# Optimization experiments

Hardware: AMD Instinct MI355X
Metric: run time of the kernel (lower is better)

The kernel has to match this reference:

```python
import jax, jax.numpy as jnp
import numpy as np

N = 50000    # nodes
E = 640000   # edges (avg degree ~12.8)
IN_NF = 64   # raw atom features
D = 96       # hidden dim
H = 4 * D    # 384
L = 4        # RPETConv layers
G = 512      # graphs in the batch
NOUT = 2


def setup_inputs():
    key = jax.random.key(0)
    ks = iter(jax.random.split(key, 64))
    def lin(shape):
        fi = shape[-2]
        return jax.random.normal(next(ks), shape, jnp.float32) / np.float32(np.sqrt(fi))
    inp = {}
    inp['x'] = jax.random.normal(next(ks), (N, IN_NF), jnp.float32)
    inp['edge_attr'] = jax.random.normal(next(ks), (E, D), jnp.float32)
    inp['emb_W1'] = lin((IN_NF, H)); inp['emb_b1'] = jnp.zeros((H,), jnp.float32)
    inp['emb_W2'] = lin((H, D));     inp['emb_b2'] = jnp.zeros((D,), jnp.float32)
    for nm in ('Wq', 'Wk', 'Wv', 'ffn_W1', 'ffn_W2'):
        inp[nm] = lin((L, D, D))
    for nm in ('bq', 'bk', 'bv', 'ffn_b1', 'ffn_b2', 'n1_b', 'n2_b'):
        inp[nm] = jnp.zeros((L, D), jnp.float32)
    inp['n1_g'] = jnp.ones((L, D), jnp.float32)
    inp['n2_g'] = jnp.ones((L, D), jnp.float32)
    inp['u_W1'] = lin((D, H)); inp['u_b1'] = jnp.zeros((H,), jnp.float32)
    inp['u_W2'] = lin((H, H)); inp['u_b2'] = jnp.zeros((H,), jnp.float32)
    inp['u_g'] = jnp.ones((H,), jnp.float32); inp['u_b'] = jnp.zeros((H,), jnp.float32)
    inp['clf_W'] = lin((H, NOUT)); inp['clf_b'] = jnp.zeros((NOUT,), jnp.float32)
    inp['rec_W1'] = lin((H, H)); inp['rec_b1'] = jnp.zeros((H,), jnp.float32)
    inp['rec_W2'] = lin((H, IN_NF)); inp['rec_b2'] = jnp.zeros((IN_NF,), jnp.float32)
    inp['edge_index'] = jax.random.randint(next(ks), (2, E), 0, N, jnp.int32)
    inp['batch_index'] = jnp.sort(jax.random.randint(next(ks), (N,), 0, G, jnp.int32))
    return inp


def _ln(x, g, b):
    # torch.nn.LayerNorm, eps=1e-5
    m = x.mean(-1, keepdims=True)
    v = ((x - m) ** 2).mean(-1, keepdims=True)
    return (x - m) * jax.lax.rsqrt(v + 1e-5) * g + b


def _forward(fs, edge_index, batch_index):
    (x, edge_attr, emb_W1, emb_b1, emb_W2, emb_b2,
     Wq, bq, Wk, bk, Wv, bv, n1_g, n1_b,
     ffn_W1, ffn_b1, ffn_W2, ffn_b2, n2_g, n2_b,
     u_W1, u_b1, u_W2, u_b2, u_g, u_b,
     clf_W, clf_b, rec_W1, rec_b1, rec_W2, rec_b2) = fs
    src, dst = edge_index[0], edge_index[1]  # PyG: x_j = x[src], x_i = x[dst]
    scale = D ** -0.5
    # atom embedding MLP
    h = jax.nn.relu(x @ emb_W1 + emb_b1) @ emb_W2 + emb_b2  # [N, D]
    for l in range(L):
        x_i = h[dst]                  # [E, D] target gather
        px = h[src] + edge_attr       # [E, D] source + relative positional edge attr
        q = x_i @ Wq[l] + bq[l]
        k = px @ Wk[l] + bk[l]
        v = px @ Wv[l] + bv[l]
        ae = jnp.exp((q * k).sum(-1) * scale)  # [E] (original uses raw exp, no max-sub)
        # faithful quirk: softmax denominator segmented over SOURCE index
        s = ae / jax.ops.segment_sum(ae, src, num_segments=N)[src]
        # aggregation (aggr='add') goes to TARGET index
        agg = jax.ops.segment_sum(s[:, None] * v, dst, num_segments=N)  # [N, D]
        h1 = _ln(h + agg, n1_g[l], n1_b[l])
        f = jax.nn.elu(h1 @ ffn_W1[l] + ffn_b1[l]) @ ffn_W2[l] + ffn_b2[l]
        h = _ln(f + h1, n2_g[l], n2_b[l])
    # updim
    u = jax.nn.leaky_relu(h @ u_W1 + u_b1, 0.01) @ u_W2 + u_b2
    u = _ln(u, u_g, u_b)              # [N, H]
    # mean readout per graph
    cnt = jnp.maximum(jax.ops.segment_sum(jnp.ones((N,), u.dtype), batch_index, num_segments=G), 1.0)
    pooled = jax.ops.segment_sum(u, batch_index, num_segments=G) / cnt[:, None]  # [G, H]
    out = pooled @ clf_W + clf_b      # [G, NOUT]
    r = jax.nn.relu(u @ rec_W1 + rec_b1) @ rec_W2 + rec_b2  # [N, IN_NF]
    return (out, r)


def reference(x, edge_attr, emb_W1, emb_b1, emb_W2, emb_b2, Wq, bq, Wk, bk, Wv, bv, n1_g, n1_b, ffn_W1, ffn_b1, ffn_W2, ffn_b2, n2_g, n2_b, u_W1, u_b1, u_W2, u_b2, u_g, u_b, clf_W, clf_b, rec_W1, rec_b1, rec_W2, rec_b2, edge_index, batch_index):
    fs = (x, edge_attr, emb_W1, emb_b1, emb_W2, emb_b2, Wq, bq, Wk, bk, Wv, bv, n1_g, n1_b,
          ffn_W1, ffn_b1, ffn_W2, ffn_b2, n2_g, n2_b, u_W1, u_b1, u_W2, u_b2, u_g, u_b,
          clf_W, clf_b, rec_W1, rec_b1, rec_W2, rec_b2)
    return _forward(fs, edge_index, batch_index)
```

## Files before the change

### kernel.cpp

```cpp
#include <hip/hip_runtime.h>
#include <math.h>

#define N_NODES 50000
#define N_EDGES 640000
#define INF_ 64
#define DD 96
#define HH 384
#define NLAYERS 4
#define NGRAPH 512
#define NOUT_ 2
#define MAXDEG 64

#define ACT_NONE 0
#define ACT_RELU 1
#define ACT_ELU 2
#define ACT_LEAKY 3

typedef unsigned int uint;
typedef unsigned short ushort;
typedef __attribute__((ext_vector_type(8))) short v8s;
typedef __attribute__((ext_vector_type(4))) float v4f;

__device__ __forceinline__ float bf_lo(uint u) { return __uint_as_float(u << 16); }
__device__ __forceinline__ float bf_hi(uint u) { return __uint_as_float(u & 0xffff0000u); }
__device__ __forceinline__ float bfs(ushort s) { return __uint_as_float(((uint)s) << 16); }
__device__ __forceinline__ ushort f2bf(float f)
{
    uint u = __float_as_uint(f);
    return (ushort)((u + 0x7fffu + ((u >> 16) & 1u)) >> 16);
}

template<int BN, int ACT, bool ACCUM, bool OUT16>
__global__ __launch_bounds__(256)
void gemm_mf(const ushort* __restrict__ A, const ushort* __restrict__ Bt,
             const float* __restrict__ bias, float* __restrict__ C32,
             ushort* __restrict__ C16, int M, int Nc, int K)
{
    const int BM = 128, LDA = 40;
    const int FN = BN / 32;
    __shared__ ushort As[BM * LDA];
    __shared__ ushort Bs[BN * LDA];
    int tid = threadIdx.x;
    int lane = tid & 63, wave = tid >> 6;
    int ln15 = lane & 15, quad = lane >> 4;
    int wm = (wave >> 1) * 64, wn = (wave & 1) * (BN / 2);
    int bm0 = blockIdx.x * BM, bn0 = blockIdx.y * BN;

    v4f acc[4][FN];
    #pragma unroll
    for (int i = 0; i < 4; i++)
        #pragma unroll
        for (int j = 0; j < FN; j++) acc[i][j] = (v4f){0.f, 0.f, 0.f, 0.f};

    for (int k0 = 0; k0 < K; k0 += 32) {
        #pragma unroll
        for (int it = 0; it < 2; it++) {
            int u = it * 256 + tid;
            int r = u >> 2, c8 = (u & 3) * 8;
            int row = bm0 + r;
            int4 v = make_int4(0, 0, 0, 0);
            if (row < M) v = *(const int4*)&A[(size_t)row * K + k0 + c8];
            *(int4*)&As[r * LDA + c8] = v;
        }
        #pragma unroll
        for (int it = 0; it < (BN * 4 + 255) / 256; it++) {
            int u = it * 256 + tid;
            if ((BN * 4) % 256 == 0 || u < BN * 4) {
                int r = u >> 2, c8 = (u & 3) * 8;
                *(int4*)&Bs[r * LDA + c8] =
                    *(const int4*)&Bt[(size_t)(bn0 + r) * K + k0 + c8];
            }
        }
        __syncthreads();
        v8s af[4], bf[FN];
        #pragma unroll
        for (int i = 0; i < 4; i++)
            af[i] = *(const v8s*)&As[(wm + i * 16 + ln15) * LDA + quad * 8];
        #pragma unroll
        for (int j = 0; j < FN; j++)
            bf[j] = *(const v8s*)&Bs[(wn + j * 16 + ln15) * LDA + quad * 8];
        #pragma unroll
        for (int i = 0; i < 4; i++)
            #pragma unroll
            for (int j = 0; j < FN; j++)
                acc[i][j] = __builtin_amdgcn_mfma_f32_16x16x32_bf16(
                    af[i], bf[j], acc[i][j], 0, 0, 0);
        __syncthreads();
    }
    #pragma unroll
    for (int i = 0; i < 4; i++) {
        #pragma unroll
        for (int j = 0; j < FN; j++) {
            int col = bn0 + wn + j * 16 + ln15;
            float bsv = bias ? bias[col] : 0.f;
            #pragma unroll
            for (int r = 0; r < 4; r++) {
                int row = bm0 + wm + i * 16 + quad * 4 + r;
                if (row >= M) continue;
                float v = acc[i][j][r] + bsv;
                if (ACCUM) v += C32[(size_t)row * Nc + col];
                if (ACT == ACT_RELU)       v = fmaxf(v, 0.f);
                else if (ACT == ACT_ELU)   v = v > 0.f ? v : expm1f(v);
                else if (ACT == ACT_LEAKY) v = v > 0.f ? v : 0.01f * v;
                if (OUT16) C16[(size_t)row * Nc + col] = f2bf(v);
                else       C32[(size_t)row * Nc + col] = v;
            }
        }
    }
}

template<bool ACC32>
__global__ __launch_bounds__(256)
void gemm_ln(const ushort* __restrict__ A, const ushort* __restrict__ Bt,
             const float* __restrict__ bias, const float* __restrict__ C32,
             const ushort* __restrict__ add16,
             const float* __restrict__ g, const float* __restrict__ beta,
             ushort* __restrict__ out, int M, int K)
{
    const int BM = 128, LDA = 40, FN = 3;
    __shared__ ushort As[BM * LDA];
    __shared__ ushort Bs[96 * LDA];
    __shared__ float2 red[2][2][64];
    int tid = threadIdx.x;
    int lane = tid & 63, wave = tid >> 6;
    int ln15 = lane & 15, quad = lane >> 4;
    int wm = (wave >> 1) * 64, wn = (wave & 1) * 48;
    int bm0 = blockIdx.x * BM;

    v4f acc[4][FN];
    #pragma unroll
    for (int i = 0; i < 4; i++)
        #pragma unroll
        for (int j = 0; j < FN; j++) acc[i][j] = (v4f){0.f, 0.f, 0.f, 0.f};

    for (int k0 = 0; k0 < K; k0 += 32) {
        #pragma unroll
        for (int it = 0; it < 2; it++) {
            int u = it * 256 + tid;
            int r = u >> 2, c8 = (u & 3) * 8;
            int row = bm0 + r;
            int4 v = make_int4(0, 0, 0, 0);
            if (row < M) v = *(const int4*)&A[(size_t)row * K + k0 + c8];
            *(int4*)&As[r * LDA + c8] = v;
        }
        #pragma unroll
        for (int it = 0; it < 2; it++) {
            int u = it * 256 + tid;
            if (u < 384) {
                int r = u >> 2, c8 = (u & 3) * 8;
                *(int4*)&Bs[r * LDA + c8] =
                    *(const int4*)&Bt[(size_t)r * K + k0 + c8];
            }
        }
        __syncthreads();
        v8s af[4], bf[FN];
        #pragma unroll
        for (int i = 0; i < 4; i++)
            af[i] = *(const v8s*)&As[(wm + i * 16 + ln15) * LDA + quad * 8];
        #pragma unroll
        for (int j = 0; j < FN; j++)
            bf[j] = *(const v8s*)&Bs[(wn + j * 16 + ln15) * LDA + quad * 8];
        #pragma unroll
        for (int i = 0; i < 4; i++)
            #pragma unroll
            for (int j = 0; j < FN; j++)
                acc[i][j] = __builtin_amdgcn_mfma_f32_16x16x32_bf16(
                    af[i], bf[j], acc[i][j], 0, 0, 0);
        __syncthreads();
    }

    float s1a[4][4], s2a[4][4];
    #pragma unroll
    for (int i = 0; i < 4; i++)
        #pragma unroll
        for (int r = 0; r < 4; r++) { s1a[i][r] = 0.f; s2a[i][r] = 0.f; }

    #pragma unroll
    for (int i = 0; i < 4; i++) {
        #pragma unroll
        for (int j = 0; j < FN; j++) {
            int col = wn + j * 16 + ln15;
            float bsv = bias ? bias[col] : 0.f;
            #pragma unroll
            for (int r = 0; r < 4; r++) {
                int row = bm0 + wm + i * 16 + quad * 4 + r;
                float v = acc[i][j][r] + bsv;
                if (row < M) {
                    if (ACC32) v += C32[(size_t)row * DD + col];
                    v += bfs(add16[(size_t)row * DD + col]);
                }
                acc[i][j][r] = v;
                s1a[i][r] += v; s2a[i][r] += v * v;
            }
        }
    }
    #pragma unroll
    for (int o = 1; o <= 8; o <<= 1) {
        #pragma unroll
        for (int i = 0; i < 4; i++)
            #pragma unroll
            for (int r = 0; r < 4; r++) {
                s1a[i][r] += __shfl_xor(s1a[i][r], o);
                s2a[i][r] += __shfl_xor(s2a[i][r], o);
            }
    }
    if (ln15 == 0) {
        #pragma unroll
        for (int i = 0; i < 4; i++)
            #pragma unroll
            for (int r = 0; r < 4; r++)
                red[wave >> 1][wave & 1][i * 16 + quad * 4 + r] =
                    make_float2(s1a[i][r], s2a[i][r]);
    }
    __syncthreads();
    float gj[FN], bj[FN];
    #pragma unroll
    for (int j = 0; j < FN; j++) {
        gj[j] = g[wn + j * 16 + ln15];
        bj[j] = beta[wn + j * 16 + ln15];
    }
    #pragma unroll
    for (int i = 0; i < 4; i++) {
        #pragma unroll
        for (int r = 0; r < 4; r++) {
            int row = bm0 + wm + i * 16 + quad * 4 + r;
            if (row >= M) continue;
            float2 o = red[wave >> 1][(wave & 1) ^ 1][i * 16 + quad * 4 + r];
            float tot1 = s1a[i][r] + o.x;
            float tot2 = s2a[i][r] + o.y;
            float mean = tot1 * (1.f / 96.f);
            float var  = tot2 * (1.f / 96.f) - mean * mean;
            float rstd = rsqrtf(var + 1e-5f);
            #pragma unroll
            for (int j = 0; j < FN; j++) {
                int col = wn + j * 16 + ln15;
                out[(size_t)row * DD + col] =
                    f2bf((acc[i][j][r] - mean) * rstd * gj[j] + bj[j]);
            }
        }
    }
}

__device__ __forceinline__ float wave_reduce_sum(float v)
{
    #pragma unroll
    for (int o = 32; o > 0; o >>= 1) v += __shfl_xor(v, o, 64);
    return v;
}

__global__ __launch_bounds__(256)
void cvt16(const float* __restrict__ in, ushort* __restrict__ out, long n)
{
    long i = ((long)blockIdx.x * 256 + threadIdx.x) * 4;
    if (i >= n) return;
    float4 v = *(const float4*)&in[i];
    ushort4 o;
    o.x = f2bf(v.x); o.y = f2bf(v.y); o.z = f2bf(v.z); o.w = f2bf(v.w);
    *(ushort4*)&out[i] = o;
}

__global__ __launch_bounds__(256)
void wqk_k(const float* __restrict__ Wq, const float* __restrict__ Wk,
           const float* __restrict__ bq, float* __restrict__ Wcat, float* __restrict__ bcat)
{
    int l = blockIdx.y;
    int idx = blockIdx.x * 256 + threadIdx.x;
    const float* wq = Wq + (size_t)l * DD * DD;
    const float* wk = Wk + (size_t)l * DD * DD;
    if (idx < DD * DD) {
        int k = idx / DD, j = idx % DD;
        float s = 0.f;
        for (int t = 0; t < DD; t++) s += wq[k * DD + t] * wk[j * DD + t];
        Wcat[(size_t)l * DD * 4 * DD + (size_t)k * 4 * DD + 288 + j] = s;
    }
    if (idx < DD) {
        int j = idx;
        float s = 0.f;
        for (int t = 0; t < DD; t++) s += bq[l * DD + t] * wk[j * DD + t];
        bcat[l * 4 * DD + 288 + j] = s;
    }
}

__global__ __launch_bounds__(256)
void pack_k(const float* __restrict__ Wq, const float* __restrict__ Wk,
            const float* __restrict__ Wv, const float* __restrict__ bq,
            const float* __restrict__ bk, const float* __restrict__ bv,
            float* __restrict__ Wcat, float* __restrict__ bcat)
{
    int idx = blockIdx.x * 256 + threadIdx.x;
    if (idx >= NLAYERS * DD * 288) return;
    int l = idx / (DD * 288);
    int rem = idx % (DD * 288);
    int k = rem / 288, n = rem % 288;
    int which = n / DD, j = n % DD;
    const float* W = which == 0 ? Wq : (which == 1 ? Wk : Wv);
    Wcat[(size_t)l * DD * 4 * DD + (size_t)k * 4 * DD + n] =
        W[(size_t)l * DD * DD + k * DD + j];
    if (k == 0) {
        const float* bb = which == 0 ? bq : (which == 1 ? bk : bv);
        bcat[l * 4 * DD + n] = bb[l * DD + j];
    }
}

#define NPACK 22
struct PackArgs {
    const float* src[NPACK];
    ushort* dst[NPACK];
    int K[NPACK], N[NPACK];
};
__global__ __launch_bounds__(256)
void packT_k(PackArgs pa)
{
    int w = blockIdx.y;
    int K = pa.K[w], N = pa.N[w];
    int idx = blockIdx.x * 256 + threadIdx.x;
    if (idx >= K * N) return;
    int n = idx / K, k = idx % K;
    pa.dst[w][(size_t)n * K + k] = f2bf(pa.src[w][(size_t)k * N + n]);
}

__global__ __launch_bounds__(256)
void scatter_k(const int* __restrict__ src, const int* __restrict__ dst,
               int* __restrict__ deg, int2* __restrict__ pe)
{
    int e = blockIdx.x * 256 + threadIdx.x;
    if (e >= N_EDGES) return;
    int d = dst[e];
    int c = atomicAdd(&deg[d], 1);
    if (c < MAXDEG) pe[(size_t)d * MAXDEG + c] = make_int2(src[e], e);
}

template<bool EA16>
__global__ __launch_bounds__(256)
void edge1w(const ushort* __restrict__ qkv16, const void* __restrict__ eaP,
            const int2* __restrict__ pe, const int* __restrict__ deg,
            float* __restrict__ ae_slot, float* __restrict__ denom, float scale)
{
    int lane = threadIdx.x & 63;
    int grp = lane >> 4, t = lane & 15;
    int d = blockIdx.x * 4 + (threadIdx.x >> 6);
    if (d >= N_NODES) return;
    int cnt = deg[d]; if (cnt > MAXDEG) cnt = MAXDEG;
    if (cnt == 0) return;
    const uint* row = (const uint*)qkv16 + (size_t)d * 192;
    uint qa = row[t], qb = row[16 + t], qc = row[32 + t];
    uint pa = row[144 + t], pb = row[160 + t], pc = row[176 + t];
    float q0l = bf_lo(qa), q0h = bf_hi(qa), q1l = bf_lo(qb), q1h = bf_hi(qb),
          q2l = bf_lo(qc), q2h = bf_hi(qc);
    float p0l = bf_lo(pa), p0h = bf_hi(pa), p1l = bf_lo(pb), p1h = bf_hi(pb),
          p2l = bf_lo(pc), p2h = bf_hi(pc);
    int2 pr = pe[(size_t)d * MAXDEG + lane];
    for (int cb = 0; cb < cnt; cb += 8) {
        float dots[2];
        int sxu[2];
        #pragma unroll
        for (int u = 0; u < 2; u++) {
            int myc = cb + u * 4 + grp;
            int cc = myc < cnt ? myc : cnt - 1;
            int sx = __shfl(pr.x, cc);
            int ex = __shfl(pr.y, cc);
            sxu[u] = sx;
            const uint* kr = (const uint*)qkv16 + (size_t)sx * 192 + 48;
            uint k0 = kr[t], k1 = kr[16 + t], k2 = kr[32 + t];
            float e0l, e0h, e1l, e1h, e2l, e2h;
            if (EA16) {
                const uint* er = (const uint*)eaP + (size_t)ex * 48;
                uint e0 = er[t], e1 = er[16 + t], e2 = er[32 + t];
                e0l = bf_lo(e0); e0h = bf_hi(e0);
                e1l = bf_lo(e1); e1h = bf_hi(e1);
                e2l = bf_lo(e2); e2h = bf_hi(e2);
            } else {
                const float* er = (const float*)eaP + (size_t)ex * DD;
                float2 f0 = *(const float2*)&er[2 * t];
                float2 f1 = *(const float2*)&er[32 + 2 * t];
                float2 f2 = *(const float2*)&er[64 + 2 * t];
                e0l = f0.x; e0h = f0.y; e1l = f1.x; e1h = f1.y;
                e2l = f2.x; e2h = f2.y;
            }
            dots[u] = q0l * bf_lo(k0) + q0h * bf_hi(k0)
                    + q1l * bf_lo(k1) + q1h * bf_hi(k1)
                    + q2l * bf_lo(k2) + q2h * bf_hi(k2)
                    + p0l * e0l + p0h * e0h + p1l * e1l + p1h * e1h
                    + p2l * e2l + p2h * e2h;
        }
        #pragma unroll
        for (int o = 8; o > 0; o >>= 1) {
            dots[0] += __shfl_xor(dots[0], o);
            dots[1] += __shfl_xor(dots[1], o);
        }
        #pragma unroll
        for (int u = 0; u < 2; u++) {
            int myc = cb + u * 4 + grp;
            if (t == 0 && myc < cnt) {
                float v = __expf(dots[u] * scale);
                ae_slot[(size_t)d * MAXDEG + myc] = v;
                atomicAdd(&denom[sxu[u]], v);
            }
        }
    }
}

template<bool EA16>
__global__ __launch_bounds__(256)
void edge2w(const ushort* __restrict__ qkv16, const void* __restrict__ eaP,
            const float* __restrict__ ae_slot, const float* __restrict__ denom,
            const int2* __restrict__ pe, const int* __restrict__ deg,
            float* __restrict__ agg, ushort* __restrict__ T16)
{
    int lane = threadIdx.x & 63;
    int grp = lane >> 4, t = lane & 15;
    int d = blockIdx.x * 4 + (threadIdx.x >> 6);
    if (d >= N_NODES) return;
    int cnt = deg[d]; if (cnt > MAXDEG) cnt = MAXDEG;
    int2 pr = pe[(size_t)d * MAXDEG + lane];
    float ar = ae_slot[(size_t)d * MAXDEG + lane];
    float a0l = 0.f, a0h = 0.f, a1l = 0.f, a1h = 0.f, a2l = 0.f, a2h = 0.f;
    float t0l = 0.f, t0h = 0.f, t1l = 0.f, t1h = 0.f, t2l = 0.f, t2h = 0.f;
    for (int cb = 0; cb < cnt; cb += 8) {
        #pragma unroll
        for (int u = 0; u < 2; u++) {
            int myc = cb + u * 4 + grp;
            int cc = myc < cnt ? myc : cnt - 1;
            int sx = __shfl(pr.x, cc);
            int ex = __shfl(pr.y, cc);
            float ae = __shfl(ar, cc);
            float w = (myc < cnt) ? ae / denom[sx] : 0.f;
            const uint* vr = (const uint*)qkv16 + (size_t)sx * 192 + 96;
            uint v0 = vr[t], v1 = vr[16 + t], v2 = vr[32 + t];
            float e0l, e0h, e1l, e1h, e2l, e2h;
            if (EA16) {
                const uint* er = (const uint*)eaP + (size_t)ex * 48;
                uint e0 = er[t], e1 = er[16 + t], e2 = er[32 + t];
                e0l = bf_lo(e0); e0h = bf_hi(e0);
                e1l = bf_lo(e1); e1h = bf_hi(e1);
                e2l = bf_lo(e2); e2h = bf_hi(e2);
            } else {
                const float* er = (const float*)eaP + (size_t)ex * DD;
                float2 f0 = *(const float2*)&er[2 * t];
                float2 f1 = *(const float2*)&er[32 + 2 * t];
                float2 f2 = *(const float2*)&er[64 + 2 * t];
                e0l = f0.x; e0h = f0.y; e1l = f1.x; e1h = f1.y;
                e2l = f2.x; e2h = f2.y;
            }
            a0l += w * bf_lo(v0); a0h += w * bf_hi(v0);
            a1l += w * bf_lo(v1); a1h += w * bf_hi(v1);
            a2l += w * bf_lo(v2); a2h += w * bf_hi(v2);
            t0l += w * e0l; t0h += w * e0h;
            t1l += w * e1l; t1h += w * e1h;
            t2l += w * e2l; t2h += w * e2h;
        }
    }
    #pragma unroll
    for (int o = 16; o <= 32; o <<= 1) {
        a0l += __shfl_xor(a0l, o); a0h += __shfl_xor(a0h, o);
        a1l += __shfl_xor(a1l, o); a1h += __shfl_xor(a1h, o);
        a2l += __shfl_xor(a2l, o); a2h += __shfl_xor(a2h, o);
        t0l += __shfl_xor(t0l, o); t0h += __shfl_xor(t0h, o);
        t1l += __shfl_xor(t1l, o); t1h += __shfl_xor(t1h, o);
        t2l += __shfl_xor(t2l, o); t2h += __shfl_xor(t2h, o);
    }
    if (grp == 0) {
        *(float2*)&agg[(size_t)d * DD + 2 * t]      = make_float2(a0l, a0h);
        *(float2*)&agg[(size_t)d * DD + 32 + 2 * t] = make_float2(a1l, a1h);
        *(float2*)&agg[(size_t)d * DD + 64 + 2 * t] = make_float2(a2l, a2h);
        uint* Tw = (uint*)T16 + (size_t)d * 48;
        Tw[t]      = ((uint)f2bf(t0h) << 16) | f2bf(t0l);
        Tw[16 + t] = ((uint)f2bf(t1h) << 16) | f2bf(t1l);
        Tw[32 + t] = ((uint)f2bf(t2h) << 16) | f2bf(t2l);
    }
}

template<int RL, int BMODE>
__global__ __launch_bounds__(256)
void ln_b(const ushort* __restrict__ a, const void* __restrict__ bP,
          const float* __restrict__ g, const float* __restrict__ beta,
          ushort* __restrict__ out, int M)
{
    int wave = threadIdx.x >> 6;
    int lane = threadIdx.x & 63;
    int row = blockIdx.x * 4 + wave;
    if (row >= M) return;
    const int NE = (RL + 63) / 64;
    float vals[NE];
    float s = 0.f;
    #pragma unroll
    for (int i = 0; i < NE; i++) {
        int j = lane + i * 64;
        float x = 0.f;
        if (j < RL) {
            x = bfs(a[(size_t)row * RL + j]);
            if (BMODE == 1) x += ((const float*)bP)[(size_t)row * RL + j];
            if (BMODE == 2) x += bfs(((const ushort*)bP)[(size_t)row * RL + j]);
        }
        vals[i] = x; s += x;
    }
    s = wave_reduce_sum(s);
    float mean = s / RL;
    float sq = 0.f;
    #pragma unroll
    for (int i = 0; i < NE; i++) {
        int j = lane + i * 64;
        if (j < RL) { float dd = vals[i] - mean; sq += dd * dd; }
    }
    sq = wave_reduce_sum(sq);
    float rstd = rsqrtf(sq / RL + 1e-5f);
    #pragma unroll
    for (int i = 0; i < NE; i++) {
        int j = lane + i * 64;
        if (j < RL)
            out[(size_t)row * RL + j] = f2bf((vals[i] - mean) * rstd * g[j] + beta[j]);
    }
}

#define PCHUNK 64
__global__ __launch_bounds__(192)
void pool2_k(const ushort* __restrict__ u, const int* __restrict__ batch,
             float* __restrict__ pooled, float* __restrict__ cnt)
{
    int j = threadIdx.x;
    int n0 = blockIdx.x * PCHUNK;
    if (n0 >= N_NODES) return;
    int n1 = n0 + PCHUNK; if (n1 > N_NODES) n1 = N_NODES;
    float a0 = 0.f, a1 = 0.f;
    int cur = batch[n0];
    int runStart = n0;
    for (int n = n0; n < n1; n++) {
        int bg = batch[n];
        if (bg != cur) {
            atomicAdd(&pooled[(size_t)cur * HH + 2 * j], a0);
            atomicAdd(&pooled[(size_t)cur * HH + 2 * j + 1], a1);
            if (j == 0) atomicAdd(&cnt[cur], (float)(n - runStart));
            a0 = 0.f; a1 = 0.f; cur = bg; runStart = n;
        }
        uint v = ((const uint*)u)[(size_t)n * 192 + j];
        a0 += bf_lo(v); a1 += bf_hi(v);
    }
    atomicAdd(&pooled[(size_t)cur * HH + 2 * j], a0);
    atomicAdd(&pooled[(size_t)cur * HH + 2 * j + 1], a1);
    if (j == 0) atomicAdd(&cnt[cur], (float)(n1 - runStart));
}

__global__ __launch_bounds__(64)
void clf_k(const float* __restrict__ pooled, const float* __restrict__ cnt,
           const float* __restrict__ W, const float* __restrict__ bcl,
           float* __restrict__ out)
{
    int g = blockIdx.x;
    int lane = threadIdx.x;
    float c = cnt[g]; c = c > 1.f ? c : 1.f;
    float inv = 1.f / c;
    float a0 = 0.f, a1 = 0.f;
    #pragma unroll
    for (int i = 0; i < 6; i++) {
        int j = lane + i * 64;
        float pv = pooled[(size_t)g * HH + j] * inv;
        a0 += pv * W[j * 2 + 0];
        a1 += pv * W[j * 2 + 1];
    }
    a0 = wave_reduce_sum(a0);
    a1 = wave_reduce_sum(a1);
    if (lane == 0) {
        out[g * 2 + 0] = a0 + bcl[0];
        out[g * 2 + 1] = a1 + bcl[1];
    }
}

extern "C" void kernel_launch(void* const* d_in, const int* in_sizes, int n_in,
                              void* d_out, int out_size, void* d_ws, size_t ws_size,
                              hipStream_t stream)
{
    const float* x       = (const float*)d_in[0];
    const float* ea      = (const float*)d_in[1];
    const float* emb_W1  = (const float*)d_in[2];
    const float* emb_b1  = (const float*)d_in[3];
    const float* emb_W2  = (const float*)d_in[4];
    const float* emb_b2  = (const float*)d_in[5];
    const float* Wq      = (const float*)d_in[6];
    const float* Wk      = (const float*)d_in[7];
    const float* Wv      = (const float*)d_in[8];
    const float* ffn_W1  = (const float*)d_in[9];
    const float* ffn_W2  = (const float*)d_in[10];
    const float* bq      = (const float*)d_in[11];
    const float* bk      = (const float*)d_in[12];
    const float* bv      = (const float*)d_in[13];
    const float* ffn_b1  = (const float*)d_in[14];
    const float* ffn_b2  = (const float*)d_in[15];
    const float* n1_b    = (const float*)d_in[16];
    const float* n2_b    = (const float*)d_in[17];
    const float* n1_g    = (const float*)d_in[18];
    const float* n2_g    = (const float*)d_in[19];
    const float* u_W1    = (const float*)d_in[20];
    const float* u_b1    = (const float*)d_in[21];
    const float* u_W2    = (const float*)d_in[22];
    const float* u_b2    = (const float*)d_in[23];
    const float* u_g     = (const float*)d_in[24];
    const float* u_bb    = (const float*)d_in[25];
    const float* clf_W   = (const float*)d_in[26];
    const float* clf_b   = (const float*)d_in[27];
    const float* rec_W1  = (const float*)d_in[28];
    const float* rec_b1  = (const float*)d_in[29];
    const float* rec_W2  = (const float*)d_in[30];
    const float* rec_b2  = (const float*)d_in[31];
    const int* edge_index = (const int*)d_in[32];
    const int* batch     = (const int*)d_in[33];
    const int* srcI = edge_index;
    const int* dstI = edge_index + N_EDGES;

    float* out   = (float*)d_out;
    float* r_out = out + NGRAPH * NOUT_;

    char* base = (char*)d_ws;
    size_t off = 0;
    auto alloc = [&](size_t bytes) -> char* {
        char* r = base + off;
        off += (bytes + 255) & ~(size_t)255;
        return r;
    };
    ushort* h16     = (ushort*)alloc((size_t)N_NODES * DD * 2);
    ushort* qkv16   = (ushort*)alloc((size_t)N_NODES * HH * 2);
    float*  agg     = (float*) alloc((size_t)N_NODES * DD * 4);
    ushort* T16     = (ushort*)alloc((size_t)N_NODES * DD * 2);
    ushort* h116    = (ushort*)alloc((size_t)N_NODES * DD * 2);
    int2*   pe      = (int2*)  alloc((size_t)N_NODES * MAXDEG * 8);
    float*  ae_slot = (float*) alloc((size_t)N_NODES * MAXDEG * 4);
    ushort* f116    = (ushort*)alloc((size_t)N_NODES * DD * 2);
    float*  denom   = (float*) alloc((size_t)N_NODES * 4);
    int*    deg     = (int*)   alloc((size_t)N_NODES * 4);
    float*  pooled  = (float*) alloc((size_t)NGRAPH * HH * 4);
    float*  cnt     = (float*) alloc(NGRAPH * 4);
    float*  Wcat    = (float*) alloc((size_t)NLAYERS * DD * 4 * DD * 4);
    float*  bcat    = (float*) alloc((size_t)NLAYERS * 4 * DD * 4);
    ushort* x16     = (ushort*)alloc((size_t)N_NODES * INF_ * 2);
    ushort* embW1T  = (ushort*)alloc((size_t)HH * INF_ * 2);
    ushort* embW2T  = (ushort*)alloc((size_t)DD * HH * 2);
    ushort* WcatT   = (ushort*)alloc((size_t)NLAYERS * HH * DD * 2);
    ushort* WvT     = (ushort*)alloc((size_t)NLAYERS * DD * DD * 2);
    ushort* fW1T    = (ushort*)alloc((size_t)NLAYERS * DD * DD * 2);
    ushort* fW2T    = (ushort*)alloc((size_t)NLAYERS * DD * DD * 2);
    ushort* uW1T    = (ushort*)alloc((size_t)HH * DD * 2);
    ushort* uW2T    = (ushort*)alloc((size_t)HH * HH * 2);
    ushort* recW1T  = (ushort*)alloc((size_t)HH * HH * 2);
    ushort* recW2T  = (ushort*)alloc((size_t)INF_ * HH * 2);
    ushort* ea16 = (ushort*)alloc((size_t)N_EDGES * DD * 2);
    bool use_ea16 = (ws_size >= off);
    const void* eaP = use_ea16 ? (const void*)ea16 : (const void*)ea;

    ushort* t16    = qkv16;
    ushort* upre16 = (ushort*)agg;
    ushort* u16    = (ushort*)pe;
    ushort* rtmp16 = qkv16;

    dim3 blk(256);
    const int GB = (N_NODES + 127) / 128;
    const float scale = 1.f / sqrtf((float)DD);

    wqk_k<<<dim3(36, NLAYERS), blk, 0, stream>>>(Wq, Wk, bq, Wcat, bcat);
    pack_k<<<(NLAYERS * DD * 288 + 255) / 256, blk, 0, stream>>>(
        Wq, Wk, Wv, bq, bk, bv, Wcat, bcat);
    PackArgs pa;
    int pi = 0;
    auto addp = [&](const float* s, ushort* d, int K, int N) {
        pa.src[pi] = s; pa.dst[pi] = d; pa.K[pi] = K; pa.N[pi] = N; pi++;
    };
    addp(emb_W1, embW1T, INF_, HH);
    addp(emb_W2, embW2T, HH, DD);
    for (int l = 0; l < NLAYERS; l++) addp(Wcat + (size_t)l * DD * 4 * DD, WcatT + (size_t)l * HH * DD, DD, HH);
    for (int l = 0; l < NLAYERS; l++) addp(Wv + (size_t)l * DD * DD, WvT + (size_t)l * DD * DD, DD, DD);
    for (int l = 0; l < NLAYERS; l++) addp(ffn_W1 + (size_t)l * DD * DD, fW1T + (size_t)l * DD * DD, DD, DD);
    for (int l = 0; l < NLAYERS; l++) addp(ffn_W2 + (size_t)l * DD * DD, fW2T + (size_t)l * DD * DD, DD, DD);
    addp(u_W1, uW1T, DD, HH);
    addp(u_W2, uW2T, HH, HH);
    addp(rec_W1, recW1T, HH, HH);
    addp(rec_W2, recW2T, HH, INF_);
    packT_k<<<dim3(576, NPACK), blk, 0, stream>>>(pa);

    cvt16<<<((size_t)N_NODES * INF_ / 4 + 255) / 256, blk, 0, stream>>>(
        x, x16, (long)N_NODES * INF_);
    if (use_ea16)
        cvt16<<<((size_t)N_EDGES * DD / 4 + 255) / 256, blk, 0, stream>>>(
            ea, ea16, (long)N_EDGES * DD);

    gemm_mf<128, ACT_RELU, false, true><<<dim3(GB, 3), blk, 0, stream>>>(
        x16, embW1T, emb_b1, nullptr, t16, N_NODES, HH, INF_);
    gemm_mf<96, ACT_NONE, false, true><<<dim3(GB, 1), blk, 0, stream>>>(
        t16, embW2T, emb_b2, nullptr, h16, N_NODES, DD, HH);

    hipMemsetAsync(deg, 0, N_NODES * sizeof(int), stream);
    scatter_k<<<(N_EDGES + 255) / 256, blk, 0, stream>>>(srcI, dstI, deg, pe);

    const int EGRID = (N_NODES + 3) / 4;
    for (int l = 0; l < NLAYERS; l++) {
        gemm_mf<128, ACT_NONE, false, true><<<dim3(GB, 3), blk, 0, stream>>>(
            h16, WcatT + (size_t)l * HH * DD, bcat + (size_t)l * 4 * DD,
            nullptr, qkv16, N_NODES, HH, DD);

        hipMemsetAsync(denom, 0, N_NODES * sizeof(float), stream);
        if (use_ea16) {
            edge1w<true><<<EGRID, blk, 0, stream>>>(
                qkv16, eaP, pe, deg, ae_slot, denom, scale);
            edge2w<true><<<EGRID, blk, 0, stream>>>(
                qkv16, eaP, ae_slot, denom, pe, deg, agg, T16);
        } else {
            edge1w<false><<<EGRID, blk, 0, stream>>>(
                qkv16, eaP, pe, deg, ae_slot, denom, scale);
            edge2w<false><<<EGRID, blk, 0, stream>>>(
                qkv16, eaP, ae_slot, denom, pe, deg, agg, T16);
        }

        gemm_ln<true><<<GB, blk, 0, stream>>>(
            T16, WvT + (size_t)l * DD * DD, nullptr, agg, h16,
            n1_g + (size_t)l * DD, n1_b + (size_t)l * DD, h116, N_NODES, DD);

        gemm_mf<96, ACT_ELU, false, true><<<dim3(GB, 1), blk, 0, stream>>>(
            h116, fW1T + (size_t)l * DD * DD, ffn_b1 + (size_t)l * DD,
            nullptr, f116, N_NODES, DD, DD);

        gemm_ln<false><<<GB, blk, 0, stream>>>(
            f116, fW2T + (size_t)l * DD * DD, ffn_b2 + (size_t)l * DD,
            nullptr, h116, n2_g + (size_t)l * DD, n2_b + (size_t)l * DD,
            h16, N_NODES, DD);
    }

    gemm_mf<128, ACT_LEAKY, false, true><<<dim3(GB, 3), blk, 0, stream>>>(
        h16, uW1T, u_b1, nullptr, t16, N_NODES, HH, DD);
    gemm_mf<128, ACT_NONE, false, true><<<dim3(GB, 3), blk, 0, stream>>>(
        t16, uW2T, u_b2, nullptr, upre16, N_NODES, HH, HH);
    ln_b<HH, 0><<<(N_NODES + 3) / 4, blk, 0, stream>>>(
        upre16, nullptr, u_g, u_bb, u16, N_NODES);

    hipMemsetAsync(pooled, 0, (size_t)(NGRAPH * HH + NGRAPH) * sizeof(float), stream);
    pool2_k<<<(N_NODES + PCHUNK - 1) / PCHUNK, 192, 0, stream>>>(u16, batch, pooled, cnt);
    clf_k<<<NGRAPH, 64, 0, stream>>>(pooled, cnt, clf_W, clf_b, out);

    gemm_mf<128, ACT_RELU, false, true><<<dim3(GB, 3), blk, 0, stream>>>(
        u16, recW1T, rec_b1, nullptr, rtmp16, N_NODES, HH, HH);
    gemm_mf<64, ACT_NONE, false, false><<<dim3(GB, 1), blk, 0, stream>>>(
        rtmp16, recW2T, rec_b2, r_out, nullptr, N_NODES, INF_, HH);
}
```

Measured before the change: 1.556 ms.

## Build CSR edge layout, permute edge features by destination, split QKV planes

Replaces the padded per-node MAXDEG slot table with a compact CSR built from a degree count, a single-block prefix scan and a scatter that records each edge's position. Edge attributes are converted to bf16 and reordered into CSR order, so the edge kernels read them contiguously per destination node. The QKV projection now writes four separate 96-wide planes instead of one interleaved 384-wide row, which shrinks the stride of the gathered K and V rows. This adds scan and permutation kernels, a serial single-block scan, and nondeterministic in-row edge order.

```diff
diff --git a/kernel.cpp b/kernel.cpp
--- a/kernel.cpp
+++ b/kernel.cpp
@@ -30,7 +30,7 @@
     return (ushort)((u + 0x7fffu + ((u >> 16) & 1u)) >> 16);
 }
 
-template<int BN, int ACT, bool ACCUM, bool OUT16>
+template<int BN, int ACT, bool ACCUM, bool OUT16, bool SPLITB = false>
 __global__ __launch_bounds__(256)
 void gemm_mf(const ushort* __restrict__ A, const ushort* __restrict__ Bt,
              const float* __restrict__ bias, float* __restrict__ C32,
@@ -102,8 +102,10 @@
                 if (ACT == ACT_RELU)       v = fmaxf(v, 0.f);
                 else if (ACT == ACT_ELU)   v = v > 0.f ? v : expm1f(v);
                 else if (ACT == ACT_LEAKY) v = v > 0.f ? v : 0.01f * v;
-                if (OUT16) C16[(size_t)row * Nc + col] = f2bf(v);
-                else       C32[(size_t)row * Nc + col] = v;
+                if (SPLITB)
+                    C16[(size_t)blockIdx.y * M * 96 + (size_t)row * 96 + (col - bn0)] = f2bf(v);
+                else if (OUT16) C16[(size_t)row * Nc + col] = f2bf(v);
+                else            C32[(size_t)row * Nc + col] = v;
             }
         }
     }
@@ -320,36 +322,95 @@
 }
 
 __global__ __launch_bounds__(256)
-void scatter_k(const int* __restrict__ src, const int* __restrict__ dst,
-               int* __restrict__ deg, int2* __restrict__ pe)
+void deg_k(const int* __restrict__ dst, int* __restrict__ deg)
+{
+    int e = blockIdx.x * 256 + threadIdx.x;
+    if (e >= N_EDGES) return;
+    atomicAdd(&deg[dst[e]], 1);
+}
+
+__global__ __launch_bounds__(1024)
+void scan_k(const int* __restrict__ deg, int* __restrict__ row_start)
+{
+    __shared__ int ps[1024];
+    int t = threadIdx.x;
+    const int CH = (N_NODES + 1023) / 1024;
+    int base = t * CH;
+    int s = 0;
+    for (int i = 0; i < CH; i++) {
+        int n = base + i;
+        if (n < N_NODES) { int d = deg[n]; s += d > MAXDEG ? MAXDEG : d; }
+    }
+    ps[t] = s;
+    __syncthreads();
+    for (int o = 1; o < 1024; o <<= 1) {
+        int v = t >= o ? ps[t - o] : 0;
+        __syncthreads();
+        ps[t] += v;
+        __syncthreads();
+    }
+    int run = t ? ps[t - 1] : 0;
+    for (int i = 0; i < CH; i++) {
+        int n = base + i;
+        if (n < N_NODES) {
+            row_start[n] = run;
+            int d = deg[n]; run += d > MAXDEG ? MAXDEG : d;
+        }
+    }
+    if (t == 1023) row_start[N_NODES] = run;
+}
+
+__global__ __launch_bounds__(256)
+void scatter2_k(const int* __restrict__ src, const int* __restrict__ dst,
+                const int* __restrict__ row_start, int* __restrict__ fill,
+                int2* __restrict__ peC, int* __restrict__ posOf)
 {
     int e = blockIdx.x * 256 + threadIdx.x;
     if (e >= N_EDGES) return;
     int d = dst[e];
-    int c = atomicAdd(&deg[d], 1);
-    if (c < MAXDEG) pe[(size_t)d * MAXDEG + c] = make_int2(src[e], e);
+    int c = atomicAdd(&fill[d], 1);
+    if (c < MAXDEG) {
+        int p = row_start[d] + c;
+        peC[p] = make_int2(src[e], e);
+        posOf[e] = p;
+    } else posOf[e] = -1;
+}
+
+__global__ __launch_bounds__(256)
+void cvt_ea_k(const float* __restrict__ ea, const int* __restrict__ posOf,
+              ushort* __restrict__ ea_s)
+{
+    long idx = (long)blockIdx.x * 256 + threadIdx.x;
+    if (idx >= (long)N_EDGES * 48) return;
+    int e = (int)(idx / 48), q = (int)(idx % 48);
+    int p = posOf[e];
+    if (p < 0) return;
+    float2 f = *(const float2*)&ea[(size_t)e * 96 + 2 * q];
+    ((uint*)ea_s)[(size_t)p * 48 + q] = ((uint)f2bf(f.y) << 16) | f2bf(f.x);
 }
 
 template<bool EA16>
 __global__ __launch_bounds__(256)
-void edge1w(const ushort* __restrict__ qkv16, const void* __restrict__ eaP,
-            const int2* __restrict__ pe, const int* __restrict__ deg,
-            float* __restrict__ ae_slot, float* __restrict__ denom, float scale)
+void edge1c(const ushort* __restrict__ qkv16, const void* __restrict__ eaP,
+            const int2* __restrict__ peC, const int* __restrict__ rsA,
+            float* __restrict__ aeC, float* __restrict__ denom, float scale)
 {
     int lane = threadIdx.x & 63;
     int grp = lane >> 4, t = lane & 15;
     int d = blockIdx.x * 4 + (threadIdx.x >> 6);
     if (d >= N_NODES) return;
-    int cnt = deg[d]; if (cnt > MAXDEG) cnt = MAXDEG;
+    int rs = rsA[d], cnt = rsA[d + 1] - rs;
     if (cnt == 0) return;
-    const uint* row = (const uint*)qkv16 + (size_t)d * 192;
-    uint qa = row[t], qb = row[16 + t], qc = row[32 + t];
-    uint pa = row[144 + t], pb = row[160 + t], pc = row[176 + t];
+    const size_t NB = (size_t)N_NODES * 48;
+    const uint* qr = (const uint*)qkv16 + (size_t)d * 48;
+    const uint* pr_ = (const uint*)qkv16 + NB * 3 + (size_t)d * 48;
+    uint qa = qr[t], qb = qr[16 + t], qc = qr[32 + t];
+    uint pa = pr_[t], pb = pr_[16 + t], pc = pr_[32 + t];
     float q0l = bf_lo(qa), q0h = bf_hi(qa), q1l = bf_lo(qb), q1h = bf_hi(qb),
           q2l = bf_lo(qc), q2h = bf_hi(qc);
     float p0l = bf_lo(pa), p0h = bf_hi(pa), p1l = bf_lo(pb), p1h = bf_hi(pb),
           p2l = bf_lo(pc), p2h = bf_hi(pc);
-    int2 pr = pe[(size_t)d * MAXDEG + lane];
+    int2 pr = peC[rs + lane];
     for (int cb = 0; cb < cnt; cb += 8) {
         float dots[2];
         int sxu[2];
@@ -358,18 +419,18 @@
             int myc = cb + u * 4 + grp;
             int cc = myc < cnt ? myc : cnt - 1;
             int sx = __shfl(pr.x, cc);
-            int ex = __shfl(pr.y, cc);
             sxu[u] = sx;
-            const uint* kr = (const uint*)qkv16 + (size_t)sx * 192 + 48;
+            const uint* kr = (const uint*)qkv16 + NB + (size_t)sx * 48;
             uint k0 = kr[t], k1 = kr[16 + t], k2 = kr[32 + t];
             float e0l, e0h, e1l, e1h, e2l, e2h;
             if (EA16) {
-                const uint* er = (const uint*)eaP + (size_t)ex * 48;
+                const uint* er = (const uint*)eaP + (size_t)(rs + cc) * 48;
                 uint e0 = er[t], e1 = er[16 + t], e2 = er[32 + t];
                 e0l = bf_lo(e0); e0h = bf_hi(e0);
                 e1l = bf_lo(e1); e1h = bf_hi(e1);
                 e2l = bf_lo(e2); e2h = bf_hi(e2);
             } else {
+                int ex = __shfl(pr.y, cc);
                 const float* er = (const float*)eaP + (size_t)ex * DD;
                 float2 f0 = *(const float2*)&er[2 * t];
                 float2 f1 = *(const float2*)&er[32 + 2 * t];
@@ -393,7 +454,7 @@
             int myc = cb + u * 4 + grp;
             if (t == 0 && myc < cnt) {
                 float v = __expf(dots[u] * scale);
-                ae_slot[(size_t)d * MAXDEG + myc] = v;
+                aeC[rs + myc] = v;
                 atomicAdd(&denom[sxu[u]], v);
             }
         }
@@ -402,18 +463,19 @@
 
 template<bool EA16>
 __global__ __launch_bounds__(256)
-void edge2w(const ushort* __restrict__ qkv16, const void* __restrict__ eaP,
-            const float* __restrict__ ae_slot, const float* __restrict__ denom,
-            const int2* __restrict__ pe, const int* __restrict__ deg,
+void edge2c(const ushort* __restrict__ qkv16, const void* __restrict__ eaP,
+            const float* __restrict__ aeC, const float* __restrict__ denom,
+            const int2* __restrict__ peC, const int* __restrict__ rsA,
             float* __restrict__ agg, ushort* __restrict__ T16)
 {
     int lane = threadIdx.x & 63;
     int grp = lane >> 4, t = lane & 15;
     int d = blockIdx.x * 4 + (threadIdx.x >> 6);
     if (d >= N_NODES) return;
-    int cnt = deg[d]; if (cnt > MAXDEG) cnt = MAXDEG;
-    int2 pr = pe[(size_t)d * MAXDEG + lane];
-    float ar = ae_slot[(size_t)d * MAXDEG + lane];
+    int rs = rsA[d], cnt = rsA[d + 1] - rs;
+    const size_t NB = (size_t)N_NODES * 48;
+    int2 pr = peC[rs + lane];
+    float ar = aeC[rs + lane];
     float a0l = 0.f, a0h = 0.f, a1l = 0.f, a1h = 0.f, a2l = 0.f, a2h = 0.f;
     float t0l = 0.f, t0h = 0.f, t1l = 0.f, t1h = 0.f, t2l = 0.f, t2h = 0.f;
     for (int cb = 0; cb < cnt; cb += 8) {
@@ -422,19 +484,19 @@
             int myc = cb + u * 4 + grp;
             int cc = myc < cnt ? myc : cnt - 1;
             int sx = __shfl(pr.x, cc);
-            int ex = __shfl(pr.y, cc);
             float ae = __shfl(ar, cc);
             float w = (myc < cnt) ? ae / denom[sx] : 0.f;
-            const uint* vr = (const uint*)qkv16 + (size_t)sx * 192 + 96;
+            const uint* vr = (const uint*)qkv16 + NB * 2 + (size_t)sx * 48;
             uint v0 = vr[t], v1 = vr[16 + t], v2 = vr[32 + t];
             float e0l, e0h, e1l, e1h, e2l, e2h;
             if (EA16) {
-                const uint* er = (const uint*)eaP + (size_t)ex * 48;
+                const uint* er = (const uint*)eaP + (size_t)(rs + cc) * 48;
                 uint e0 = er[t], e1 = er[16 + t], e2 = er[32 + t];
                 e0l = bf_lo(e0); e0h = bf_hi(e0);
                 e1l = bf_lo(e1); e1h = bf_hi(e1);
                 e2l = bf_lo(e2); e2h = bf_hi(e2);
             } else {
+                int ex = __shfl(pr.y, cc);
                 const float* er = (const float*)eaP + (size_t)ex * DD;
                 float2 f0 = *(const float2*)&er[2 * t];
                 float2 f1 = *(const float2*)&er[32 + 2 * t];
@@ -621,11 +683,15 @@
     float*  agg     = (float*) alloc((size_t)N_NODES * DD * 4);
     ushort* T16     = (ushort*)alloc((size_t)N_NODES * DD * 2);
     ushort* h116    = (ushort*)alloc((size_t)N_NODES * DD * 2);
-    int2*   pe      = (int2*)  alloc((size_t)N_NODES * MAXDEG * 8);
-    float*  ae_slot = (float*) alloc((size_t)N_NODES * MAXDEG * 4);
+    int2*   peC     = (int2*)  alloc((size_t)(N_EDGES + 64) * 8);
+    float*  aeC     = (float*) alloc((size_t)(N_EDGES + 64) * 4);
     ushort* f116    = (ushort*)alloc((size_t)N_NODES * DD * 2);
     float*  denom   = (float*) alloc((size_t)N_NODES * 4);
-    int*    deg     = (int*)   alloc((size_t)N_NODES * 4);
+    int*    degfill = (int*)   alloc((size_t)2 * N_NODES * 4);
+    int*    deg     = degfill;
+    int*    fill    = degfill + N_NODES;
+    int*    row_start = (int*) alloc((size_t)(N_NODES + 2) * 4);
+    int*    posOf   = (int*)   alloc((size_t)N_EDGES * 4);
     float*  pooled  = (float*) alloc((size_t)NGRAPH * HH * 4);
     float*  cnt     = (float*) alloc(NGRAPH * 4);
     float*  Wcat    = (float*) alloc((size_t)NLAYERS * DD * 4 * DD * 4);
@@ -641,13 +707,14 @@
     ushort* uW2T    = (ushort*)alloc((size_t)HH * HH * 2);
     ushort* recW1T  = (ushort*)alloc((size_t)HH * HH * 2);
     ushort* recW2T  = (ushort*)alloc((size_t)INF_ * HH * 2);
-    ushort* ea16 = (ushort*)alloc((size_t)N_EDGES * DD * 2);
+    size_t off_base = off;
+    ushort* ea_s    = (ushort*)alloc((size_t)(N_EDGES + 64) * DD * 2);
     bool use_ea16 = (ws_size >= off);
-    const void* eaP = use_ea16 ? (const void*)ea16 : (const void*)ea;
+    const void* eaP = use_ea16 ? (const void*)ea_s : (const void*)ea;
 
     ushort* t16    = qkv16;
     ushort* upre16 = (ushort*)agg;
-    ushort* u16    = (ushort*)pe;
+    ushort* u16    = use_ea16 ? ea_s : (ushort*)(base + off_base);
     ushort* rtmp16 = qkv16;
 
     dim3 blk(256);
@@ -674,37 +741,40 @@
     addp(rec_W2, recW2T, HH, INF_);
     packT_k<<<dim3(576, NPACK), blk, 0, stream>>>(pa);
 
+    hipMemsetAsync(degfill, 0, (size_t)2 * N_NODES * sizeof(int), stream);
+    deg_k<<<(N_EDGES + 255) / 256, blk, 0, stream>>>(dstI, deg);
+    scan_k<<<1, 1024, 0, stream>>>(deg, row_start);
+    scatter2_k<<<(N_EDGES + 255) / 256, blk, 0, stream>>>(
+        srcI, dstI, row_start, fill, peC, posOf);
+
     cvt16<<<((size_t)N_NODES * INF_ / 4 + 255) / 256, blk, 0, stream>>>(
         x, x16, (long)N_NODES * INF_);
     if (use_ea16)
-        cvt16<<<((size_t)N_EDGES * DD / 4 + 255) / 256, blk, 0, stream>>>(
-            ea, ea16, (long)N_EDGES * DD);
+        cvt_ea_k<<<(int)(((long)N_EDGES * 48 + 255) / 256), blk, 0, stream>>>(
+            ea, posOf, ea_s);
 
     gemm_mf<128, ACT_RELU, false, true><<<dim3(GB, 3), blk, 0, stream>>>(
         x16, embW1T, emb_b1, nullptr, t16, N_NODES, HH, INF_);
     gemm_mf<96, ACT_NONE, false, true><<<dim3(GB, 1), blk, 0, stream>>>(
         t16, embW2T, emb_b2, nullptr, h16, N_NODES, DD, HH);
 
-    hipMemsetAsync(deg, 0, N_NODES * sizeof(int), stream);
-    scatter_k<<<(N_EDGES + 255) / 256, blk, 0, stream>>>(srcI, dstI, deg, pe);
-
     const int EGRID = (N_NODES + 3) / 4;
     for (int l = 0; l < NLAYERS; l++) {
-        gemm_mf<128, ACT_NONE, false, true><<<dim3(GB, 3), blk, 0, stream>>>(
+        gemm_mf<96, ACT_NONE, false, true, true><<<dim3(GB, 4), blk, 0, stream>>>(
             h16, WcatT + (size_t)l * HH * DD, bcat + (size_t)l * 4 * DD,
-            nullptr, qkv16, N_NODES, HH, DD);
+            nullptr, qkv16, N_NODES, 96, DD);
 
         hipMemsetAsync(denom, 0, N_NODES * sizeof(float), stream);
         if (use_ea16) {
-            edge1w<true><<<EGRID, blk, 0, stream>>>(
-                qkv16, eaP, pe, deg, ae_slot, denom, scale);
-            edge2w<true><<<EGRID, blk, 0, stream>>>(
-                qkv16, eaP, ae_slot, denom, pe, deg, agg, T16);
+            edge1c<true><<<EGRID, blk, 0, stream>>>(
+                qkv16, eaP, peC, row_start, aeC, denom, scale);
+            edge2c<true><<<EGRID, blk, 0, stream>>>(
+                qkv16, eaP, aeC, denom, peC, row_start, agg, T16);
         } else {
-            edge1w<false><<<EGRID, blk, 0, stream>>>(
-                qkv16, eaP, pe, deg, ae_slot, denom, scale);
-            edge2w<false><<<EGRID, blk, 0, stream>>>(
-                qkv16, eaP, ae_slot, denom, pe, deg, agg, T16);
+            edge1c<false><<<EGRID, blk, 0, stream>>>(
+                qkv16, eaP, peC, row_start, aeC, denom, scale);
+            edge2c<false><<<EGRID, blk, 0, stream>>>(
+                qkv16, eaP, aeC, denom, peC, row_start, agg, T16);
         }
 
         gemm_ln<true><<<GB, blk, 0, stream>>>(
```

Result: slower. 1.630 ms (+4.7%).
